# Kernel optimization log

Measured on AMD Instinct MI355X. Metric: run time of the kernel, lower is better.

The kernel has to match this reference:

```python
import jax, jax.numpy as jnp
import numpy as np

M = 262144          # total lanes
N_GROUPS = 32768    # unique obstacle ids (static; original uses torch.unique)
H = 64              # lane_hidden_size
I = 64              # lane_info_enc_size
F = 64              # lane_future_enc_size
SOFT_ARGMAX_DEGREE = 1.0


def setup_inputs() -> dict:
    key = jax.random.key(0)
    k = jax.random.split(key, 8)
    lane_ht = jax.random.normal(k[0], (M, H), jnp.float32)
    lane_info_enc = jax.random.normal(k[1], (M, I), jnp.float32)
    lane_future_enc = jax.random.normal(k[2], (M, F), jnp.float32)
    # sorted group ids covering every group (8 lanes per obstacle)
    same_obstacle_mask = jnp.sort(jnp.arange(M, dtype=jnp.int32) % N_GROUPS).reshape(M, 1)
    # lane_scoring_mlp params: Linear(128->16) + ReLU + Linear(16->1)
    W1 = jax.random.normal(k[3], (H + I, 16), jnp.float32) * 0.05
    b1 = jnp.zeros((16,), jnp.float32)
    W2 = jax.random.normal(k[4], (16, 1), jnp.float32) * 0.05
    b2 = jnp.zeros((1,), jnp.float32)
    return {"lane_ht": lane_ht, "lane_info_enc": lane_info_enc,
            "lane_future_enc": lane_future_enc,
            "W1": W1, "b1": b1, "W2": W2, "b2": b2,
            "same_obstacle_mask": same_obstacle_mask}


def reference(lane_ht, lane_info_enc, lane_future_enc, W1, b1, W2, b2, same_obstacle_mask):
    seg = same_obstacle_mask.reshape(-1)                       # [M] int group ids
    # per-lane score via small MLP
    x = jnp.concatenate([lane_ht, lane_info_enc], axis=1)      # [M, 128]
    h = jax.nn.relu(x @ W1 + b1)                               # [M, 16]
    score = (h @ W2 + b2).reshape(-1) * SOFT_ARGMAX_DEGREE     # [M]
    # per-group (segment) softmax -- exact math of the dense MxN min/max/exp/sum emulation
    smax = jax.lax.stop_gradient(
        jax.ops.segment_max(score, seg, num_segments=N_GROUPS))  # [N]
    e = jnp.exp(score - smax[seg])                             # [M]
    denom = jax.ops.segment_sum(e, seg, num_segments=N_GROUPS)  # [N]
    prob = e / denom[seg]                                      # [M]
    # softmax-weighted per-group pooling of concatenated encodings
    total = jnp.concatenate([lane_ht, lane_info_enc, lane_future_enc], axis=1)  # [M, 192]
    return jax.ops.segment_sum(total * prob[:, None], seg, num_segments=N_GROUPS)  # [N, 192]
```

## Files before the change

### kernel.cpp

```cpp
#include <hip/hip_runtime.h>


__global__ __launch_bounds__(64) void lane_attn_kernel(
    const float* __restrict__ ht,
    const float* __restrict__ info,
    const float* __restrict__ fut,
    const float* __restrict__ W1,
    const float* __restrict__ b1,
    const float* __restrict__ W2,
    const float* __restrict__ b2,
    const int*   __restrict__ seg,
    float*       __restrict__ out)
{
    const int t    = threadIdx.x;
    const int base = blockIdx.x * 64;
    const int lane = base + t;

    float h[16];
#pragma unroll
    for (int j = 0; j < 16; ++j) h[j] = b1[j];

    const float4* htp = (const float4*)(ht   + (size_t)lane * 64);
    const float4* inp = (const float4*)(info + (size_t)lane * 64);

#pragma unroll 4
    for (int k4 = 0; k4 < 16; ++k4) {
        float4 v = htp[k4];
#pragma unroll
        for (int j = 0; j < 16; ++j) {
            h[j] = fmaf(v.x, W1[(k4 * 4 + 0) * 16 + j], h[j]);
            h[j] = fmaf(v.y, W1[(k4 * 4 + 1) * 16 + j], h[j]);
            h[j] = fmaf(v.z, W1[(k4 * 4 + 2) * 16 + j], h[j]);
            h[j] = fmaf(v.w, W1[(k4 * 4 + 3) * 16 + j], h[j]);
        }
    }
#pragma unroll 4
    for (int k4 = 0; k4 < 16; ++k4) {
        float4 v = inp[k4];
#pragma unroll
        for (int j = 0; j < 16; ++j) {
            h[j] = fmaf(v.x, W1[(64 + k4 * 4 + 0) * 16 + j], h[j]);
            h[j] = fmaf(v.y, W1[(64 + k4 * 4 + 1) * 16 + j], h[j]);
            h[j] = fmaf(v.z, W1[(64 + k4 * 4 + 2) * 16 + j], h[j]);
            h[j] = fmaf(v.w, W1[(64 + k4 * 4 + 3) * 16 + j], h[j]);
        }
    }

    float score = b2[0];
#pragma unroll
    for (int j = 0; j < 16; ++j)
        score = fmaf(fmaxf(h[j], 0.0f), W2[j], score);

    float m = score;
    m = fmaxf(m, __shfl_xor(m, 1));
    m = fmaxf(m, __shfl_xor(m, 2));
    m = fmaxf(m, __shfl_xor(m, 4));
    float e = __expf(score - m);
    float s = e;
    s += __shfl_xor(s, 1);
    s += __shfl_xor(s, 2);
    s += __shfl_xor(s, 4);
    const float prob = e / s;

    const int c = t;
    for (int gg = 0; gg < 8; ++gg) {
        const int r0  = base + gg * 8;
        const int gid = seg[r0];
        float a0 = 0.0f, a1 = 0.0f, a2 = 0.0f;
#pragma unroll
        for (int i = 0; i < 8; ++i) {
            const float  p = __shfl(prob, gg * 8 + i);
            const size_t r = (size_t)(r0 + i) * 64;
            a0 = fmaf(p, ht[r + c],   a0);
            a1 = fmaf(p, info[r + c], a1);
            a2 = fmaf(p, fut[r + c],  a2);
        }
        float* o = out + (size_t)gid * 192;
        o[c]       = a0;
        o[64 + c]  = a1;
        o[128 + c] = a2;
    }
}

extern "C" void kernel_launch(void* const* d_in, const int* in_sizes, int n_in,
                              void* d_out, int out_size, void* d_ws, size_t ws_size,
                              hipStream_t stream) {
    const float* ht   = (const float*)d_in[0];
    const float* info = (const float*)d_in[1];
    const float* fut  = (const float*)d_in[2];
    const float* W1   = (const float*)d_in[3];
    const float* b1   = (const float*)d_in[4];
    const float* W2   = (const float*)d_in[5];
    const float* b2   = (const float*)d_in[6];
    const int*   seg  = (const int*)d_in[7];
    float*       out  = (float*)d_out;

    const int M = in_sizes[7];
    const int blocks = M / 64;

    lane_attn_kernel<<<blocks, 64, 0, stream>>>(ht, info, fut, W1, b1, W2, b2,
                                                seg, out);
}
```

Before: 220.1 us.

## Split MLP reduction across two wavefronts per block with LDS combine

Each block now runs two wavefronts: one computes the hidden-layer partial sums from lane_ht and the other from lane_info_enc. The partials are combined through shared memory, and each wave then scores and pools half of the 64 lanes (4 groups each). This halves the serial per-thread FMA chain and raises parallelism and occupancy, in exchange for an LDS round trip and a block-wide barrier.

```diff
diff --git a/kernel.cpp b/kernel.cpp
--- a/kernel.cpp
+++ b/kernel.cpp
@@ -1,7 +1,7 @@
 #include <hip/hip_runtime.h>
 
 
-__global__ __launch_bounds__(64) void lane_attn_kernel(
+__global__ __launch_bounds__(128, 8) void lane_attn_kernel(
     const float* __restrict__ ht,
     const float* __restrict__ info,
     const float* __restrict__ fut,
@@ -12,44 +12,43 @@
     const int*   __restrict__ seg,
     float*       __restrict__ out)
 {
-    const int t    = threadIdx.x;
+    const int t    = threadIdx.x & 63;
+    const int w    = __builtin_amdgcn_readfirstlane(threadIdx.x >> 6);
     const int base = blockIdx.x * 64;
-    const int lane = base + t;
+
+    __shared__ float hpart[2][64][17];
 
     float h[16];
 #pragma unroll
-    for (int j = 0; j < 16; ++j) h[j] = b1[j];
+    for (int j = 0; j < 16; ++j) h[j] = w ? 0.0f : b1[j];
 
-    const float4* htp = (const float4*)(ht   + (size_t)lane * 64);
-    const float4* inp = (const float4*)(info + (size_t)lane * 64);
+    const float*  src = w ? info : ht;
+    const float*  w1  = W1 + w * (64 * 16);
+    const float4* p   = (const float4*)(src + (size_t)(base + t) * 64);
 
-#pragma unroll 4
+#pragma unroll 8
     for (int k4 = 0; k4 < 16; ++k4) {
-        float4 v = htp[k4];
+        float4 v = p[k4];
 #pragma unroll
         for (int j = 0; j < 16; ++j) {
-            h[j] = fmaf(v.x, W1[(k4 * 4 + 0) * 16 + j], h[j]);
-            h[j] = fmaf(v.y, W1[(k4 * 4 + 1) * 16 + j], h[j]);
-            h[j] = fmaf(v.z, W1[(k4 * 4 + 2) * 16 + j], h[j]);
-            h[j] = fmaf(v.w, W1[(k4 * 4 + 3) * 16 + j], h[j]);
-        }
-    }
-#pragma unroll 4
-    for (int k4 = 0; k4 < 16; ++k4) {
-        float4 v = inp[k4];
-#pragma unroll
-        for (int j = 0; j < 16; ++j) {
-            h[j] = fmaf(v.x, W1[(64 + k4 * 4 + 0) * 16 + j], h[j]);
-            h[j] = fmaf(v.y, W1[(64 + k4 * 4 + 1) * 16 + j], h[j]);
-            h[j] = fmaf(v.z, W1[(64 + k4 * 4 + 2) * 16 + j], h[j]);
-            h[j] = fmaf(v.w, W1[(64 + k4 * 4 + 3) * 16 + j], h[j]);
+            h[j] = fmaf(v.x, w1[(k4 * 4 + 0) * 16 + j], h[j]);
+            h[j] = fmaf(v.y, w1[(k4 * 4 + 1) * 16 + j], h[j]);
+            h[j] = fmaf(v.z, w1[(k4 * 4 + 2) * 16 + j], h[j]);
+            h[j] = fmaf(v.w, w1[(k4 * 4 + 3) * 16 + j], h[j]);
         }
     }
 
+#pragma unroll
+    for (int j = 0; j < 16; ++j) hpart[w][t][j] = h[j];
+    __syncthreads();
+
+    const int lr = w * 32 + (t & 31);
     float score = b2[0];
 #pragma unroll
-    for (int j = 0; j < 16; ++j)
-        score = fmaf(fmaxf(h[j], 0.0f), W2[j], score);
+    for (int j = 0; j < 16; ++j) {
+        const float hj = hpart[0][lr][j] + hpart[1][lr][j];
+        score = fmaf(fmaxf(hj, 0.0f), W2[j], score);
+    }
 
     float m = score;
     m = fmaxf(m, __shfl_xor(m, 1));
@@ -63,17 +62,17 @@
     const float prob = e / s;
 
     const int c = t;
-    for (int gg = 0; gg < 8; ++gg) {
-        const int r0  = base + gg * 8;
+    for (int gg = 0; gg < 4; ++gg) {
+        const int r0  = base + w * 32 + gg * 8;
         const int gid = seg[r0];
         float a0 = 0.0f, a1 = 0.0f, a2 = 0.0f;
 #pragma unroll
         for (int i = 0; i < 8; ++i) {
-            const float  p = __shfl(prob, gg * 8 + i);
-            const size_t r = (size_t)(r0 + i) * 64;
-            a0 = fmaf(p, ht[r + c],   a0);
-            a1 = fmaf(p, info[r + c], a1);
-            a2 = fmaf(p, fut[r + c],  a2);
+            const float  pb = __shfl(prob, gg * 8 + i);
+            const size_t r  = (size_t)(r0 + i) * 64;
+            a0 = fmaf(pb, ht[r + c],   a0);
+            a1 = fmaf(pb, info[r + c], a1);
+            a2 = fmaf(pb, fut[r + c],  a2);
         }
         float* o = out + (size_t)gid * 192;
         o[c]       = a0;
@@ -98,6 +97,6 @@
     const int M = in_sizes[7];
     const int blocks = M / 64;
 
-    lane_attn_kernel<<<blocks, 64, 0, stream>>>(ht, info, fut, W1, b1, W2, b2,
-                                                seg, out);
+    lane_attn_kernel<<<blocks, 128, 0, stream>>>(ht, info, fut, W1, b1, W2, b2,
+                                                 seg, out);
 }
```

Measured after the change: 215.8 us. -2.0%, faster.
